# Performance work log

Hardware: AMD Instinct MI355X
Metric: run time of the kernel (lower is better)

Reference implementation:

```python
import jax, jax.numpy as jnp
import numpy as np

THRESHOLD = 0.99
B, M, H = 8, 2048, 1024


def setup_inputs():
    key = jax.random.key(0)
    ks = jax.random.split(key, 8)
    x = jax.random.normal(ks[0], (B, M, H), jnp.float32)
    run = jax.random.randint(ks[1], (B, M), 0, 2) > 0
    acc_p = jax.random.uniform(ks[2], (B, M, 1), jnp.float32) * 0.6
    weighted_h = jax.random.normal(ks[3], (B, M, H), jnp.float32)
    remainders = jnp.zeros((B, M, 1), jnp.float32)
    exit_ = jnp.zeros((B, M, 1), jnp.int32)
    pad_h = jax.random.normal(ks[4], (H,), jnp.float32)
    p_w = jax.random.normal(ks[5], (H, 1), jnp.float32) / np.sqrt(H)
    p_b = jnp.zeros((1,), jnp.float32)
    return {"x": x, "run": run, "acc_p": acc_p, "weighted_h": weighted_h,
            "remainders": remainders, "exit_": exit_, "updates": 3,
            "pad_h": pad_h, "p_w": p_w, "p_b": p_b}


def _unpack(x, run):
    # restore left-packed x to full [B, M, H] with zeros at non-run slots
    rank = jnp.cumsum(run, axis=1) - 1                      # [B, M] position in packed row
    g = jnp.take_along_axis(x, jnp.maximum(rank, 0)[..., None], axis=1)
    return jnp.where(run[..., None], g, jnp.zeros((), x.dtype))


def _pack(h, run, pad_h):
    # left-pack run tokens; tail slots get the pad vector (pad_ semantics).
    # Static-shape variant of torch pack: output is [B, M, H] (max_ <= M).
    order = jnp.argsort(~run, axis=1)                       # stable sort: run tokens first
    packed = jnp.take_along_axis(h, order[..., None], axis=1)
    counts = jnp.sum(run, axis=1, keepdims=True)            # [B, 1]
    valid = jnp.arange(run.shape[1])[None, :] < counts      # [B, M]
    return jnp.where(valid[..., None], packed, pad_h[None, None, :])


def reference(x, run, acc_p, weighted_h, remainders, exit_, updates, pad_h, p_w, p_b):
    runf = run[..., None].astype(x.dtype)                   # [B, M, 1]
    h = _unpack(x, run)                                     # [B, M, H]
    p = jax.nn.sigmoid(jnp.einsum('bmh,ho->bmo', h, p_w) + p_b) * runf
    mask_continue = ((acc_p + p) < THRESHOLD) & run[..., None]
    mask_exit = (~mask_continue) & run[..., None]
    mc = mask_continue.astype(x.dtype)
    me = mask_exit.astype(x.dtype)
    update = p * mc + (1.0 - acc_p) * me
    weighted_h_new = h * update + weighted_h
    run_new = run & mask_continue[..., 0]
    acc_p_new = acc_p + update * mc
    remainders_new = remainders + (1.0 - acc_p_new) * me
    updates_new = updates + 1
    exit_new = exit_ + updates_new * mask_exit.astype(exit_.dtype)
    h_packed = _pack(h, run_new, pad_h)
    return (h_packed, weighted_h_new, acc_p_new, remainders_new, run_new, exit_new)
```

## Files before the change

### kernel.cpp

```cpp
#include <hip/hip_runtime.h>

#define BB 8
#define MM 2048
#define HH 1024
#define THRESH 0.99f
#define BMH ((size_t)BB * MM * HH)
#define BM (BB * MM)

__global__ __launch_bounds__(256) void scan_kernel(const int* __restrict__ flags,
                                                   int* __restrict__ rank,
                                                   int* __restrict__ counts) {
    __shared__ int ssum[256];
    const int b = blockIdx.x;
    const int t = threadIdx.x;
    const int* row = flags + b * MM;

    int local[8];
    int s = 0;
#pragma unroll
    for (int i = 0; i < 8; ++i) {
        local[i] = (row[t * 8 + i] != 0) ? 1 : 0;
        s += local[i];
    }
    ssum[t] = s;
    __syncthreads();

    for (int off = 1; off < 256; off <<= 1) {
        int v = 0;
        if (t >= off) v = ssum[t - off];
        __syncthreads();
        if (t >= off) ssum[t] += v;
        __syncthreads();
    }

    int running = (t == 0) ? 0 : ssum[t - 1];
    int* rrow = rank + b * MM;
#pragma unroll
    for (int i = 0; i < 8; ++i) {
        running += local[i];
        rrow[t * 8 + i] = running - 1;
    }
    if (t == 255 && counts != nullptr) counts[b] = ssum[255];
}

__global__ __launch_bounds__(256) void main_kernel(
    const float* __restrict__ x, const int* __restrict__ run,
    const float* __restrict__ acc_p, const float* __restrict__ weighted_h,
    const float* __restrict__ remainders, const int* __restrict__ exit_,
    const int* __restrict__ updates, const float* __restrict__ p_w,
    const float* __restrict__ p_b, const int* __restrict__ rank,
    float* __restrict__ out_wh, float* __restrict__ out_accp,
    float* __restrict__ out_rem, float* __restrict__ out_run,
    float* __restrict__ out_exit, int* __restrict__ run_new_i) {
    const int wave = threadIdx.x >> 6;
    const int lane = threadIdx.x & 63;
    const int t = blockIdx.x * 4 + wave;
    const int b = t >> 11;

    const bool r = (run[t] != 0);
    const float* hrow = nullptr;
    float dot = 0.f;
    if (r) {
        const int src = rank[t];
        hrow = x + ((size_t)(b * MM + src)) * HH;
#pragma unroll
        for (int j = 0; j < 4; ++j) {
            const int idx = j * 256 + lane * 4;
            const float4 hv = *(const float4*)(hrow + idx);
            const float4 wv = *(const float4*)(p_w + idx);
            dot += hv.x * wv.x + hv.y * wv.y + hv.z * wv.z + hv.w * wv.w;
        }
    }
#pragma unroll
    for (int off = 32; off > 0; off >>= 1) dot += __shfl_xor(dot, off, 64);

    const float p = r ? (1.f / (1.f + expf(-(dot + p_b[0])))) : 0.f;
    const float ap = acc_p[t];
    const bool mc = r && ((ap + p) < THRESH);
    const bool me = r && !mc;
    const float update = mc ? p : (me ? (1.f - ap) : 0.f);
    const float ap_new = mc ? (ap + p) : ap;

    const float* whrow = weighted_h + (size_t)t * HH;
    float* orow = out_wh + (size_t)t * HH;
#pragma unroll
    for (int j = 0; j < 4; ++j) {
        const int idx = j * 256 + lane * 4;
        const float4 wv = *(const float4*)(whrow + idx);
        float4 hv = make_float4(0.f, 0.f, 0.f, 0.f);
        if (r) hv = *(const float4*)(hrow + idx);
        float4 o;
        o.x = hv.x * update + wv.x;
        o.y = hv.y * update + wv.y;
        o.z = hv.z * update + wv.z;
        o.w = hv.w * update + wv.w;
        *(float4*)(orow + idx) = o;
    }

    if (lane == 0) {
        out_accp[t] = ap_new;
        out_rem[t] = remainders[t] + (me ? (1.f - ap_new) : 0.f);
        out_run[t] = mc ? 1.f : 0.f;
        out_exit[t] = (float)(exit_[t] + (me ? (updates[0] + 1) : 0));
        run_new_i[t] = mc ? 1 : 0;
    }
}

__global__ __launch_bounds__(256) void pack_kernel(
    const float* __restrict__ x, const float* __restrict__ pad_h,
    const int* __restrict__ rank, const int* __restrict__ run_new_i,
    const int* __restrict__ rank2, const int* __restrict__ counts,
    float* __restrict__ h_packed) {
    const int wave = threadIdx.x >> 6;
    const int lane = threadIdx.x & 63;
    const int t = blockIdx.x * 4 + wave;
    const int b = t >> 11;
    const int m = t & (MM - 1);
    const int cnt = counts[b];

    if (run_new_i[t] != 0) {
        const int dst = rank2[t];
        const float* src = x + ((size_t)(b * MM + rank[t])) * HH;
        float* out = h_packed + ((size_t)(b * MM + dst)) * HH;
#pragma unroll
        for (int j = 0; j < 4; ++j) {
            const int idx = j * 256 + lane * 4;
            *(float4*)(out + idx) = *(const float4*)(src + idx);
        }
    }
    if (m >= cnt) {
        float* out = h_packed + (size_t)t * HH;
#pragma unroll
        for (int j = 0; j < 4; ++j) {
            const int idx = j * 256 + lane * 4;
            *(float4*)(out + idx) = *(const float4*)(pad_h + idx);
        }
    }
}

extern "C" void kernel_launch(void* const* d_in, const int* in_sizes, int n_in,
                              void* d_out, int out_size, void* d_ws, size_t ws_size,
                              hipStream_t stream) {
    const float* x          = (const float*)d_in[0];
    const int*   run        = (const int*)d_in[1];
    const float* acc_p      = (const float*)d_in[2];
    const float* weighted_h = (const float*)d_in[3];
    const float* remainders = (const float*)d_in[4];
    const int*   exit_      = (const int*)d_in[5];
    const int*   updates    = (const int*)d_in[6];
    const float* pad_h      = (const float*)d_in[7];
    const float* p_w        = (const float*)d_in[8];
    const float* p_b        = (const float*)d_in[9];

    float* out = (float*)d_out;
    float* out_hpacked = out;
    float* out_wh      = out + BMH;
    float* out_accp    = out + 2 * BMH;
    float* out_rem     = out_accp + BM;
    float* out_run     = out_rem + BM;
    float* out_exit    = out_run + BM;

    int* rank      = (int*)d_ws;
    int* run_new_i = rank + BM;
    int* rank2     = run_new_i + BM;
    int* counts    = rank2 + BM;

    scan_kernel<<<BB, 256, 0, stream>>>(run, rank, nullptr);

    main_kernel<<<BM / 4, 256, 0, stream>>>(x, run, acc_p, weighted_h, remainders,
                                            exit_, updates, p_w, p_b, rank,
                                            out_wh, out_accp, out_rem, out_run,
                                            out_exit, run_new_i);

    scan_kernel<<<BB, 256, 0, stream>>>(run_new_i, rank2, counts);

    pack_kernel<<<BM / 4, 256, 0, stream>>>(x, pad_h, rank, run_new_i, rank2,
                                            counts, out_hpacked);
}
```

Before: 57.60 us.

## Split dot pass from fused weighted-h and pack copy pass; shuffle-based scan

Restructures the pipeline so the first pass only computes per-token halting probabilities and scalar outputs, storing the update factor in workspace. A second heavy kernel then reads each x row once and writes both the weighted_h output and the packed copy, so x is not re-read in a separate pack kernel. Both big kernels now use grid-stride loops with a fixed block count, and the scan uses wave shuffles instead of a barrier-heavy shared-memory scan. The cost is an extra read of x in the dot pass plus a small update workspace, and the ordering still needs the second scan between passes.

```diff
diff --git a/kernel.cpp b/kernel.cpp
--- a/kernel.cpp
+++ b/kernel.cpp
@@ -6,13 +6,16 @@
 #define THRESH 0.99f
 #define BMH ((size_t)BB * MM * HH)
 #define BM (BB * MM)
+#define NBLK 2048
 
 __global__ __launch_bounds__(256) void scan_kernel(const int* __restrict__ flags,
                                                    int* __restrict__ rank,
                                                    int* __restrict__ counts) {
-    __shared__ int ssum[256];
+    __shared__ int wsum[4];
     const int b = blockIdx.x;
     const int t = threadIdx.x;
+    const int wave = t >> 6;
+    const int lane = t & 63;
     const int* row = flags + b * MM;
 
     int local[8];
@@ -22,118 +25,116 @@
         local[i] = (row[t * 8 + i] != 0) ? 1 : 0;
         s += local[i];
     }
-    ssum[t] = s;
+    int inc = s;
+#pragma unroll
+    for (int off = 1; off < 64; off <<= 1) {
+        int v = __shfl_up(inc, off, 64);
+        if (lane >= off) inc += v;
+    }
+    if (lane == 63) wsum[wave] = inc;
     __syncthreads();
+    int woff = 0;
+#pragma unroll
+    for (int w = 0; w < 4; ++w) woff += (w < wave) ? wsum[w] : 0;
 
-    for (int off = 1; off < 256; off <<= 1) {
-        int v = 0;
-        if (t >= off) v = ssum[t - off];
-        __syncthreads();
-        if (t >= off) ssum[t] += v;
-        __syncthreads();
-    }
-
-    int running = (t == 0) ? 0 : ssum[t - 1];
+    int running = woff + inc - s;
     int* rrow = rank + b * MM;
 #pragma unroll
     for (int i = 0; i < 8; ++i) {
         running += local[i];
         rrow[t * 8 + i] = running - 1;
     }
-    if (t == 255 && counts != nullptr) counts[b] = ssum[255];
+    if (t == 255 && counts != nullptr) counts[b] = wsum[0] + wsum[1] + wsum[2] + wsum[3];
 }
 
-__global__ __launch_bounds__(256) void main_kernel(
+__global__ __launch_bounds__(256) void dot_kernel(
     const float* __restrict__ x, const int* __restrict__ run,
-    const float* __restrict__ acc_p, const float* __restrict__ weighted_h,
-    const float* __restrict__ remainders, const int* __restrict__ exit_,
-    const int* __restrict__ updates, const float* __restrict__ p_w,
-    const float* __restrict__ p_b, const int* __restrict__ rank,
-    float* __restrict__ out_wh, float* __restrict__ out_accp,
-    float* __restrict__ out_rem, float* __restrict__ out_run,
-    float* __restrict__ out_exit, int* __restrict__ run_new_i) {
+    const float* __restrict__ acc_p, const float* __restrict__ remainders,
+    const int* __restrict__ exit_, const int* __restrict__ updates,
+    const float* __restrict__ p_w, const float* __restrict__ p_b,
+    const int* __restrict__ rank,
+    float* __restrict__ out_accp, float* __restrict__ out_rem,
+    float* __restrict__ out_run, float* __restrict__ out_exit,
+    int* __restrict__ run_new_i, float* __restrict__ update_ws) {
     const int wave = threadIdx.x >> 6;
     const int lane = threadIdx.x & 63;
-    const int t = blockIdx.x * 4 + wave;
-    const int b = t >> 11;
 
-    const bool r = (run[t] != 0);
-    const float* hrow = nullptr;
-    float dot = 0.f;
-    if (r) {
-        const int src = rank[t];
-        hrow = x + ((size_t)(b * MM + src)) * HH;
+    for (int t = blockIdx.x * 4 + wave; t < BM; t += NBLK * 4) {
+        const int b = t >> 11;
+        const bool r = (run[t] != 0);
+        float dot = 0.f;
+        if (r) {
+            const float* hrow = x + ((size_t)(b * MM + rank[t])) * HH;
+#pragma unroll
+            for (int j = 0; j < 4; ++j) {
+                const int idx = j * 256 + lane * 4;
+                const float4 hv = *(const float4*)(hrow + idx);
+                const float4 wv = *(const float4*)(p_w + idx);
+                dot += hv.x * wv.x + hv.y * wv.y + hv.z * wv.z + hv.w * wv.w;
+            }
+        }
+#pragma unroll
+        for (int off = 32; off > 0; off >>= 1) dot += __shfl_xor(dot, off, 64);
+
+        if (lane == 0) {
+            const float p = r ? (1.f / (1.f + expf(-(dot + p_b[0])))) : 0.f;
+            const float ap = acc_p[t];
+            const bool mc = r && ((ap + p) < THRESH);
+            const bool me = r && !mc;
+            const float update = mc ? p : (me ? (1.f - ap) : 0.f);
+            const float ap_new = mc ? (ap + p) : ap;
+            out_accp[t] = ap_new;
+            out_rem[t] = remainders[t] + (me ? (1.f - ap_new) : 0.f);
+            out_run[t] = mc ? 1.f : 0.f;
+            out_exit[t] = (float)(exit_[t] + (me ? (updates[0] + 1) : 0));
+            run_new_i[t] = mc ? 1 : 0;
+            update_ws[t] = update;
+        }
+    }
+}
+
+__global__ __launch_bounds__(256) void heavy_kernel(
+    const float* __restrict__ x, const float* __restrict__ weighted_h,
+    const float* __restrict__ pad_h, const int* __restrict__ run,
+    const int* __restrict__ rank, const int* __restrict__ run_new_i,
+    const int* __restrict__ rank2, const int* __restrict__ counts,
+    const float* __restrict__ update_ws,
+    float* __restrict__ out_wh, float* __restrict__ h_packed) {
+    const int wave = threadIdx.x >> 6;
+    const int lane = threadIdx.x & 63;
+
+    for (int t = blockIdx.x * 4 + wave; t < BM; t += NBLK * 4) {
+        const int b = t >> 11;
+        const int m = t & (MM - 1);
+        const bool r = (run[t] != 0);
+        const bool rn = (run_new_i[t] != 0);
+        const float upd = update_ws[t];
+        const float* xrow = r ? (x + ((size_t)(b * MM + rank[t])) * HH) : nullptr;
+        float* dst = rn ? (h_packed + ((size_t)(b * MM + rank2[t])) * HH) : nullptr;
+        const float* whrow = weighted_h + (size_t)t * HH;
+        float* orow = out_wh + (size_t)t * HH;
+
 #pragma unroll
         for (int j = 0; j < 4; ++j) {
             const int idx = j * 256 + lane * 4;
-            const float4 hv = *(const float4*)(hrow + idx);
-            const float4 wv = *(const float4*)(p_w + idx);
-            dot += hv.x * wv.x + hv.y * wv.y + hv.z * wv.z + hv.w * wv.w;
+            const float4 wv = *(const float4*)(whrow + idx);
+            float4 hv = make_float4(0.f, 0.f, 0.f, 0.f);
+            if (r) hv = *(const float4*)(xrow + idx);
+            float4 o;
+            o.x = hv.x * upd + wv.x;
+            o.y = hv.y * upd + wv.y;
+            o.z = hv.z * upd + wv.z;
+            o.w = hv.w * upd + wv.w;
+            *(float4*)(orow + idx) = o;
+            if (rn) *(float4*)(dst + idx) = hv;
         }
-    }
+        if (m >= counts[b]) {
+            float* prow = h_packed + (size_t)t * HH;
 #pragma unroll
-    for (int off = 32; off > 0; off >>= 1) dot += __shfl_xor(dot, off, 64);
-
-    const float p = r ? (1.f / (1.f + expf(-(dot + p_b[0])))) : 0.f;
-    const float ap = acc_p[t];
-    const bool mc = r && ((ap + p) < THRESH);
-    const bool me = r && !mc;
-    const float update = mc ? p : (me ? (1.f - ap) : 0.f);
-    const float ap_new = mc ? (ap + p) : ap;
-
-    const float* whrow = weighted_h + (size_t)t * HH;
-    float* orow = out_wh + (size_t)t * HH;
-#pragma unroll
-    for (int j = 0; j < 4; ++j) {
-        const int idx = j * 256 + lane * 4;
-        const float4 wv = *(const float4*)(whrow + idx);
-        float4 hv = make_float4(0.f, 0.f, 0.f, 0.f);
-        if (r) hv = *(const float4*)(hrow + idx);
-        float4 o;
-        o.x = hv.x * update + wv.x;
-        o.y = hv.y * update + wv.y;
-        o.z = hv.z * update + wv.z;
-        o.w = hv.w * update + wv.w;
-        *(float4*)(orow + idx) = o;
-    }
-
-    if (lane == 0) {
-        out_accp[t] = ap_new;
-        out_rem[t] = remainders[t] + (me ? (1.f - ap_new) : 0.f);
-        out_run[t] = mc ? 1.f : 0.f;
-        out_exit[t] = (float)(exit_[t] + (me ? (updates[0] + 1) : 0));
-        run_new_i[t] = mc ? 1 : 0;
-    }
-}
-
-__global__ __launch_bounds__(256) void pack_kernel(
-    const float* __restrict__ x, const float* __restrict__ pad_h,
-    const int* __restrict__ rank, const int* __restrict__ run_new_i,
-    const int* __restrict__ rank2, const int* __restrict__ counts,
-    float* __restrict__ h_packed) {
-    const int wave = threadIdx.x >> 6;
-    const int lane = threadIdx.x & 63;
-    const int t = blockIdx.x * 4 + wave;
-    const int b = t >> 11;
-    const int m = t & (MM - 1);
-    const int cnt = counts[b];
-
-    if (run_new_i[t] != 0) {
-        const int dst = rank2[t];
-        const float* src = x + ((size_t)(b * MM + rank[t])) * HH;
-        float* out = h_packed + ((size_t)(b * MM + dst)) * HH;
-#pragma unroll
-        for (int j = 0; j < 4; ++j) {
-            const int idx = j * 256 + lane * 4;
-            *(float4*)(out + idx) = *(const float4*)(src + idx);
-        }
-    }
-    if (m >= cnt) {
-        float* out = h_packed + (size_t)t * HH;
-#pragma unroll
-        for (int j = 0; j < 4; ++j) {
-            const int idx = j * 256 + lane * 4;
-            *(float4*)(out + idx) = *(const float4*)(pad_h + idx);
+            for (int j = 0; j < 4; ++j) {
+                const int idx = j * 256 + lane * 4;
+                *(float4*)(prow + idx) = *(const float4*)(pad_h + idx);
+            }
         }
     }
 }
@@ -160,20 +161,21 @@
     float* out_run     = out_rem + BM;
     float* out_exit    = out_run + BM;
 
-    int* rank      = (int*)d_ws;
-    int* run_new_i = rank + BM;
-    int* rank2     = run_new_i + BM;
-    int* counts    = rank2 + BM;
+    int*   rank      = (int*)d_ws;
+    int*   run_new_i = rank + BM;
+    int*   rank2     = run_new_i + BM;
+    int*   counts    = rank2 + BM;
+    float* update_ws = (float*)(counts + 64);
 
     scan_kernel<<<BB, 256, 0, stream>>>(run, rank, nullptr);
 
-    main_kernel<<<BM / 4, 256, 0, stream>>>(x, run, acc_p, weighted_h, remainders,
-                                            exit_, updates, p_w, p_b, rank,
-                                            out_wh, out_accp, out_rem, out_run,
-                                            out_exit, run_new_i);
+    dot_kernel<<<NBLK, 256, 0, stream>>>(x, run, acc_p, remainders, exit_, updates,
+                                         p_w, p_b, rank, out_accp, out_rem,
+                                         out_run, out_exit, run_new_i, update_ws);
 
     scan_kernel<<<BB, 256, 0, stream>>>(run_new_i, rank2, counts);
 
-    pack_kernel<<<BM / 4, 256, 0, stream>>>(x, pad_h, rank, run_new_i, rank2,
-                                            counts, out_hpacked);
+    heavy_kernel<<<NBLK, 256, 0, stream>>>(x, weighted_h, pad_h, run, rank,
+                                           run_new_i, rank2, counts, update_ws,
+                                           out_wh, out_hpacked);
 }
```

Result: slower. 61.21 us (+6.3%).

## Fuse prefix scans into compute kernels, cutting launches from four to two

Applied to the files above, without the earlier changes.

Removes the two standalone per-batch scan kernels. Each block now recomputes its prefix count of run flags by reducing the row up to its chunk, then runs the main and pack work on 16 tokens. This also keeps the gathered h row in registers instead of reloading it for the weighted_h update. In exchange, every block rereads the run flags of its row, which is redundant work, and the blocks cover 16 tokens instead of 4.

```diff
diff --git a/kernel.cpp b/kernel.cpp
--- a/kernel.cpp
+++ b/kernel.cpp
@@ -6,134 +6,175 @@
 #define THRESH 0.99f
 #define BMH ((size_t)BB * MM * HH)
 #define BM (BB * MM)
-
-__global__ __launch_bounds__(256) void scan_kernel(const int* __restrict__ flags,
-                                                   int* __restrict__ rank,
-                                                   int* __restrict__ counts) {
-    __shared__ int ssum[256];
-    const int b = blockIdx.x;
-    const int t = threadIdx.x;
-    const int* row = flags + b * MM;
-
-    int local[8];
-    int s = 0;
-#pragma unroll
-    for (int i = 0; i < 8; ++i) {
-        local[i] = (row[t * 8 + i] != 0) ? 1 : 0;
-        s += local[i];
-    }
-    ssum[t] = s;
-    __syncthreads();
-
-    for (int off = 1; off < 256; off <<= 1) {
-        int v = 0;
-        if (t >= off) v = ssum[t - off];
-        __syncthreads();
-        if (t >= off) ssum[t] += v;
-        __syncthreads();
-    }
-
-    int running = (t == 0) ? 0 : ssum[t - 1];
-    int* rrow = rank + b * MM;
-#pragma unroll
-    for (int i = 0; i < 8; ++i) {
-        running += local[i];
-        rrow[t * 8 + i] = running - 1;
-    }
-    if (t == 255 && counts != nullptr) counts[b] = ssum[255];
-}
-
-__global__ __launch_bounds__(256) void main_kernel(
+#define CHUNK 16
+#define NBLK (BM / CHUNK)
+
+__global__ __launch_bounds__(256) void phase1_kernel(
     const float* __restrict__ x, const int* __restrict__ run,
     const float* __restrict__ acc_p, const float* __restrict__ weighted_h,
     const float* __restrict__ remainders, const int* __restrict__ exit_,
     const int* __restrict__ updates, const float* __restrict__ p_w,
-    const float* __restrict__ p_b, const int* __restrict__ rank,
+    const float* __restrict__ p_b,
     float* __restrict__ out_wh, float* __restrict__ out_accp,
     float* __restrict__ out_rem, float* __restrict__ out_run,
-    float* __restrict__ out_exit, int* __restrict__ run_new_i) {
-    const int wave = threadIdx.x >> 6;
-    const int lane = threadIdx.x & 63;
-    const int t = blockIdx.x * 4 + wave;
-    const int b = t >> 11;
-
-    const bool r = (run[t] != 0);
-    const float* hrow = nullptr;
-    float dot = 0.f;
-    if (r) {
-        const int src = rank[t];
-        hrow = x + ((size_t)(b * MM + src)) * HH;
+    float* __restrict__ out_exit, int* __restrict__ run_new_i,
+    int* __restrict__ rank_ws) {
+    __shared__ int red[256];
+    __shared__ int cflag[CHUNK];
+    __shared__ int crank[CHUNK];
+
+    const int t0 = blockIdx.x * CHUNK;
+    const int b  = t0 >> 11;
+    const int m0 = t0 & (MM - 1);
+    const int* rrow = run + b * MM;
+    const int tid = threadIdx.x;
+
+    int s = 0;
+    for (int i = tid; i < m0; i += 256) s += (rrow[i] != 0) ? 1 : 0;
+    red[tid] = s;
+    __syncthreads();
+#pragma unroll
+    for (int off = 128; off > 0; off >>= 1) {
+        if (tid < off) red[tid] += red[tid + off];
+        __syncthreads();
+    }
+    if (tid == 0) {
+        int base = red[0];
+#pragma unroll
+        for (int i = 0; i < CHUNK; ++i) {
+            const int f = (rrow[m0 + i] != 0) ? 1 : 0;
+            cflag[i] = f;
+            base += f;
+            crank[i] = base - 1;
+            rank_ws[t0 + i] = base - 1;
+        }
+    }
+    __syncthreads();
+
+    const int wave = tid >> 6;
+    const int lane = tid & 63;
+#pragma unroll
+    for (int q = 0; q < 4; ++q) {
+        const int ti = wave * 4 + q;
+        const int t  = t0 + ti;
+        const bool r = (cflag[ti] != 0);
+        float4 hv[4];
+        float dot = 0.f;
+        if (r) {
+            const float* xrow = x + ((size_t)(b * MM + crank[ti])) * HH;
+#pragma unroll
+            for (int j = 0; j < 4; ++j) {
+                const int idx = j * 256 + lane * 4;
+                hv[j] = *(const float4*)(xrow + idx);
+                const float4 wv = *(const float4*)(p_w + idx);
+                dot += hv[j].x * wv.x + hv[j].y * wv.y + hv[j].z * wv.z + hv[j].w * wv.w;
+            }
+        } else {
+#pragma unroll
+            for (int j = 0; j < 4; ++j) hv[j] = make_float4(0.f, 0.f, 0.f, 0.f);
+        }
+#pragma unroll
+        for (int off = 32; off > 0; off >>= 1) dot += __shfl_xor(dot, off, 64);
+
+        const float p = r ? (1.f / (1.f + expf(-(dot + p_b[0])))) : 0.f;
+        const float ap = acc_p[t];
+        const bool mc = r && ((ap + p) < THRESH);
+        const bool me = r && !mc;
+        const float upd = mc ? p : (me ? (1.f - ap) : 0.f);
+        const float ap_new = mc ? (ap + p) : ap;
+
+        const float* whrow = weighted_h + (size_t)t * HH;
+        float* orow = out_wh + (size_t)t * HH;
 #pragma unroll
         for (int j = 0; j < 4; ++j) {
             const int idx = j * 256 + lane * 4;
-            const float4 hv = *(const float4*)(hrow + idx);
-            const float4 wv = *(const float4*)(p_w + idx);
-            dot += hv.x * wv.x + hv.y * wv.y + hv.z * wv.z + hv.w * wv.w;
-        }
-    }
-#pragma unroll
-    for (int off = 32; off > 0; off >>= 1) dot += __shfl_xor(dot, off, 64);
-
-    const float p = r ? (1.f / (1.f + expf(-(dot + p_b[0])))) : 0.f;
-    const float ap = acc_p[t];
-    const bool mc = r && ((ap + p) < THRESH);
-    const bool me = r && !mc;
-    const float update = mc ? p : (me ? (1.f - ap) : 0.f);
-    const float ap_new = mc ? (ap + p) : ap;
-
-    const float* whrow = weighted_h + (size_t)t * HH;
-    float* orow = out_wh + (size_t)t * HH;
-#pragma unroll
-    for (int j = 0; j < 4; ++j) {
-        const int idx = j * 256 + lane * 4;
-        const float4 wv = *(const float4*)(whrow + idx);
-        float4 hv = make_float4(0.f, 0.f, 0.f, 0.f);
-        if (r) hv = *(const float4*)(hrow + idx);
-        float4 o;
-        o.x = hv.x * update + wv.x;
-        o.y = hv.y * update + wv.y;
-        o.z = hv.z * update + wv.z;
-        o.w = hv.w * update + wv.w;
-        *(float4*)(orow + idx) = o;
-    }
-
-    if (lane == 0) {
-        out_accp[t] = ap_new;
-        out_rem[t] = remainders[t] + (me ? (1.f - ap_new) : 0.f);
-        out_run[t] = mc ? 1.f : 0.f;
-        out_exit[t] = (float)(exit_[t] + (me ? (updates[0] + 1) : 0));
-        run_new_i[t] = mc ? 1 : 0;
+            const float4 wv = *(const float4*)(whrow + idx);
+            float4 o;
+            o.x = hv[j].x * upd + wv.x;
+            o.y = hv[j].y * upd + wv.y;
+            o.z = hv[j].z * upd + wv.z;
+            o.w = hv[j].w * upd + wv.w;
+            *(float4*)(orow + idx) = o;
+        }
+        if (lane == 0) {
+            out_accp[t] = ap_new;
+            out_rem[t]  = remainders[t] + (me ? (1.f - ap_new) : 0.f);
+            out_run[t]  = mc ? 1.f : 0.f;
+            out_exit[t] = (float)(exit_[t] + (me ? (updates[0] + 1) : 0));
+            run_new_i[t] = mc ? 1 : 0;
+        }
     }
 }
 
-__global__ __launch_bounds__(256) void pack_kernel(
+__global__ __launch_bounds__(256) void phase2_kernel(
     const float* __restrict__ x, const float* __restrict__ pad_h,
-    const int* __restrict__ rank, const int* __restrict__ run_new_i,
-    const int* __restrict__ rank2, const int* __restrict__ counts,
+    const int* __restrict__ run_new_i, const int* __restrict__ rank_ws,
     float* __restrict__ h_packed) {
-    const int wave = threadIdx.x >> 6;
-    const int lane = threadIdx.x & 63;
-    const int t = blockIdx.x * 4 + wave;
-    const int b = t >> 11;
-    const int m = t & (MM - 1);
-    const int cnt = counts[b];
-
-    if (run_new_i[t] != 0) {
-        const int dst = rank2[t];
-        const float* src = x + ((size_t)(b * MM + rank[t])) * HH;
-        float* out = h_packed + ((size_t)(b * MM + dst)) * HH;
-#pragma unroll
-        for (int j = 0; j < 4; ++j) {
-            const int idx = j * 256 + lane * 4;
-            *(float4*)(out + idx) = *(const float4*)(src + idx);
-        }
-    }
-    if (m >= cnt) {
-        float* out = h_packed + (size_t)t * HH;
-#pragma unroll
-        for (int j = 0; j < 4; ++j) {
-            const int idx = j * 256 + lane * 4;
-            *(float4*)(out + idx) = *(const float4*)(pad_h + idx);
+    __shared__ int redp[256];
+    __shared__ int reda[256];
+    __shared__ int cflag[CHUNK];
+    __shared__ int crank2[CHUNK];
+    __shared__ int scount;
+
+    const int t0 = blockIdx.x * CHUNK;
+    const int b  = t0 >> 11;
+    const int m0 = t0 & (MM - 1);
+    const int* nrow = run_new_i + b * MM;
+    const int tid = threadIdx.x;
+
+    int sp = 0, sa = 0;
+#pragma unroll
+    for (int k = 0; k < MM / 256; ++k) {
+        const int i = tid + k * 256;
+        const int f = (nrow[i] != 0) ? 1 : 0;
+        sa += f;
+        if (i < m0) sp += f;
+    }
+    redp[tid] = sp;
+    reda[tid] = sa;
+    __syncthreads();
+#pragma unroll
+    for (int off = 128; off > 0; off >>= 1) {
+        if (tid < off) { redp[tid] += redp[tid + off]; reda[tid] += reda[tid + off]; }
+        __syncthreads();
+    }
+    if (tid == 0) {
+        int base = redp[0];
+#pragma unroll
+        for (int i = 0; i < CHUNK; ++i) {
+            const int f = (nrow[m0 + i] != 0) ? 1 : 0;
+            cflag[i] = f;
+            base += f;
+            crank2[i] = base - 1;
+        }
+        scount = reda[0];
+    }
+    __syncthreads();
+
+    const int wave = tid >> 6;
+    const int lane = tid & 63;
+    const int cnt = scount;
+#pragma unroll
+    for (int q = 0; q < 4; ++q) {
+        const int ti = wave * 4 + q;
+        const int t  = t0 + ti;
+        const int m  = m0 + ti;
+        if (cflag[ti] != 0) {
+            const float* src = x + ((size_t)(b * MM + rank_ws[t])) * HH;
+            float* dst = h_packed + ((size_t)(b * MM + crank2[ti])) * HH;
+#pragma unroll
+            for (int j = 0; j < 4; ++j) {
+                const int idx = j * 256 + lane * 4;
+                *(float4*)(dst + idx) = *(const float4*)(src + idx);
+            }
+        }
+        if (m >= cnt) {
+            float* prow = h_packed + (size_t)t * HH;
+#pragma unroll
+            for (int j = 0; j < 4; ++j) {
+                const int idx = j * 256 + lane * 4;
+                *(float4*)(prow + idx) = *(const float4*)(pad_h + idx);
+            }
         }
     }
 }
@@ -160,20 +201,14 @@
     float* out_run     = out_rem + BM;
     float* out_exit    = out_run + BM;
 
-    int* rank      = (int*)d_ws;
-    int* run_new_i = rank + BM;
-    int* rank2     = run_new_i + BM;
-    int* counts    = rank2 + BM;
-
-    scan_kernel<<<BB, 256, 0, stream>>>(run, rank, nullptr);
-
-    main_kernel<<<BM / 4, 256, 0, stream>>>(x, run, acc_p, weighted_h, remainders,
-                                            exit_, updates, p_w, p_b, rank,
+    int* run_new_i = (int*)d_ws;
+    int* rank_ws   = run_new_i + BM;
+
+    phase1_kernel<<<NBLK, 256, 0, stream>>>(x, run, acc_p, weighted_h, remainders,
+                                            exit_, updates, p_w, p_b,
                                             out_wh, out_accp, out_rem, out_run,
-                                            out_exit, run_new_i);
-
-    scan_kernel<<<BB, 256, 0, stream>>>(run_new_i, rank2, counts);
-
-    pack_kernel<<<BM / 4, 256, 0, stream>>>(x, pad_h, rank, run_new_i, rank2,
-                                            counts, out_hpacked);
+                                            out_exit, run_new_i, rank_ws);
+
+    phase2_kernel<<<NBLK, 256, 0, stream>>>(x, pad_h, run_new_i, rank_ws,
+                                            out_hpacked);
 }
```

New measurement: 53.15 us. 1.08x faster.
